# Kernel tuning notes

Hardware: AMD Instinct MI355X
Metric: run time of the kernel (lower is better)

The kernel has to match this reference:

```python
import jax, jax.numpy as jnp
import numpy as np

B, L, D, F = 1, 4096, 4096, 11008
# (start, end, side): side 0 = vision expert, side 1 = language expert.
# Mirrors merge_section_size over alternating contiguous vision/language token ranges.
SEGMENTS = [(0, 1024, 0), (1024, 2048, 1), (2048, 3072, 0), (3072, 4096, 1)]


def setup_inputs() -> dict:
    key = jax.random.key(0)
    ks = jax.random.split(key, 7)
    s = 0.02  # weight init scale
    hidden_states = jax.random.normal(ks[0], (B, L, D), jnp.float32)
    tt = np.zeros((B, L), np.int32)
    for a, b, side in SEGMENTS:
        tt[:, a:b] = side
    token_type_ids = jnp.asarray(tt)
    lg_w = jax.random.normal(ks[1], (D, F), jnp.float32) * s
    lu_w = jax.random.normal(ks[2], (D, F), jnp.float32) * s
    ld_w = jax.random.normal(ks[3], (F, D), jnp.float32) * s
    vg_w = jax.random.normal(ks[4], (D, F), jnp.float32) * s
    vu_w = jax.random.normal(ks[5], (D, F), jnp.float32) * s
    vd_w = jax.random.normal(ks[6], (F, D), jnp.float32) * s
    return {
        'hidden_states': hidden_states,
        'token_type_ids': token_type_ids,
        'lg_w': lg_w, 'lu_w': lu_w, 'ld_w': ld_w,
        'vg_w': vg_w, 'vu_w': vu_w, 'vd_w': vd_w,
    }


def _swiglu_mlp(x, gw, uw, dw):
    # x: [B, T, D] -> [B, T, D]; down(silu(gate(x)) * up(x))
    h = jax.nn.silu(jnp.einsum('btd,df->btf', x, gw)) * jnp.einsum('btd,df->btf', x, uw)
    return jnp.einsum('btf,fd->btd', h, dw)


def reference(hidden_states, token_type_ids, lg_w, lu_w, ld_w, vg_w, vu_w, vd_w):
    # Split-dispatch over static contiguous segments, then concat along seq dim.
    outs = []
    for a, b, side in SEGMENTS:
        seg = hidden_states[:, a:b, :]
        if side == 1:
            outs.append(_swiglu_mlp(seg, lg_w, lu_w, ld_w))
        else:
            outs.append(_swiglu_mlp(seg, vg_w, vu_w, vd_w))
    return jnp.concatenate(outs, axis=1)
```

## Files before the change

### kernel.cpp

```cpp
#include <hip/hip_runtime.h>
#include <math.h>

typedef unsigned short u16;
typedef short s16x8 __attribute__((ext_vector_type(8)));
typedef float f32x4 __attribute__((ext_vector_type(4)));

#define GLOAD16(gp, lp)                                                        \
  __builtin_amdgcn_global_load_lds(                                            \
      (const __attribute__((address_space(1))) void*)(gp),                     \
      (__attribute__((address_space(3))) void*)(lp), 16, 0, 0)

__device__ __forceinline__ u16 f2bf(float f) {
  union { float f; unsigned u; } v; v.f = f;
  unsigned r = v.u + 0x7fffu + ((v.u >> 16) & 1u);
  return (u16)(r >> 16);
}

__global__ __launch_bounds__(256) void cvt_x_kernel(const float* __restrict__ in,
                                                    u16* __restrict__ out) {
  size_t i = ((size_t)blockIdx.x * 256 + threadIdx.x) * 8;
  float4 a = *(const float4*)(in + i);
  float4 b = *(const float4*)(in + i + 4);
  s16x8 v;
  v[0] = (short)f2bf(a.x); v[1] = (short)f2bf(a.y);
  v[2] = (short)f2bf(a.z); v[3] = (short)f2bf(a.w);
  v[4] = (short)f2bf(b.x); v[5] = (short)f2bf(b.y);
  v[6] = (short)f2bf(b.z); v[7] = (short)f2bf(b.w);
  *(s16x8*)(out + i) = v;
}

__global__ __launch_bounds__(256) void transpose_cvt_kernel(
    const float* __restrict__ in0, const float* __restrict__ in1,
    const float* __restrict__ in2, const float* __restrict__ in3,
    const float* __restrict__ in4, const float* __restrict__ in5,
    u16* __restrict__ o01, u16* __restrict__ o23,
    u16* __restrict__ o4, u16* __restrict__ o5) {
  __shared__ float s[64 * 65];
  const int mat = blockIdx.y;
  const float* in; u16* out;
  switch (mat) {
    case 0: in = in0; out = o01; break;
    case 1: in = in1; out = o01; break;
    case 2: in = in2; out = o23; break;
    case 3: in = in3; out = o23; break;
    case 4: in = in4; out = o4; break;
    default: in = in5; out = o5; break;
  }
  const int R = (mat < 4) ? 4096 : 11008;
  const int C = (mat < 4) ? 11008 : 4096;
  const int nTc = C >> 6;
  const int tr = blockIdx.x / nTc, tc = blockIdx.x - tr * nTc;
  const int r0 = tr << 6, c0 = tc << 6;
  const int t = threadIdx.x;
#pragma unroll
  for (int p = 0; p < 4; ++p) {
    const int lr = p * 16 + (t >> 4);
    const int lc = (t & 15) * 4;
    float4 v = *(const float4*)(in + (size_t)(r0 + lr) * C + (c0 + lc));
    float* sp = &s[lr * 65 + lc];
    sp[0] = v.x; sp[1] = v.y; sp[2] = v.z; sp[3] = v.w;
  }
  __syncthreads();
#pragma unroll
  for (int q = 0; q < 2; ++q) {
    const int oc = q * 32 + (t >> 3);
    const int orr = (t & 7) * 8;
    s16x8 v;
#pragma unroll
    for (int i = 0; i < 8; ++i) v[i] = (short)f2bf(s[(orr + i) * 65 + oc]);
    const int f = c0 + oc;
    size_t orow;
    if (mat < 4) orow = (size_t)((f >> 4) << 5) + ((mat & 1) << 4) + (f & 15);
    else         orow = (size_t)f;
    *(s16x8*)(out + orow * R + (r0 + orr)) = v;
  }
}

template <int KB, int EPI>
__global__ __launch_bounds__(512, 1) void gemm256(
    const u16* __restrict__ A, const u16* __restrict__ Bl,
    const u16* __restrict__ Bv, const int* __restrict__ tt,
    void* __restrict__ OutP) {
  constexpr int NK = KB / 128;
  constexpr int L = NK / 2;
  __shared__ u16 sA[2][2][128][64];
  __shared__ u16 sB[2][2][128][64];

  const int nwg = gridDim.x;
  const int bid = blockIdx.x;
  const int wg = (bid & 7) * (nwg >> 3) + (bid >> 3);
  const int mT = wg & 15;
  const int nT = wg >> 4;

  const int t = threadIdx.x;
  const int lane = t & 63;
  const int rlo = lane & 15;
  const int hi = lane >> 4;
  const int wn = (t >> 6) & 3;
  const int wm = (t >> 8) & 1;

  const int side = tt[mT << 8];
  const u16* B = side ? Bl : Bv;

  const int rowq = t >> 3;
  const int gsw = ((t & 7) ^ (rowq & 7)) << 4;
  const char* srcA = (const char*)A + (size_t)(mT * 256 + rowq) * KB + gsw;
  const char* srcB = (const char*)B + (size_t)(nT * 256 + rowq) * KB + gsw;
  char* ldsA = (char*)&sA[0][0][0][0];
  char* ldsB = (char*)&sB[0][0][0][0];
  const int woff = (t & 448) << 4;

#define STG_A(d, h, kt)                                                        \
  do {                                                                         \
    GLOAD16(srcA + (size_t)((h) * 128) * KB + (kt) * 128,                      \
            ldsA + (d) * 32768 + (h) * 16384 + woff);                          \
    GLOAD16(srcA + (size_t)((h) * 128 + 64) * KB + (kt) * 128,                 \
            ldsA + (d) * 32768 + (h) * 16384 + 8192 + woff);                   \
  } while (0)
#define STG_B(d, h, kt)                                                        \
  do {                                                                         \
    GLOAD16(srcB + (size_t)((h) * 128) * KB + (kt) * 128,                      \
            ldsB + (d) * 32768 + (h) * 16384 + woff);                          \
    GLOAD16(srcB + (size_t)((h) * 128 + 64) * KB + (kt) * 128,                 \
            ldsB + (d) * 32768 + (h) * 16384 + 8192 + woff);                   \
  } while (0)

  const int cxa = (hi ^ (rlo & 7)) << 4;
  const int cxb = ((4 + hi) ^ (rlo & 7)) << 4;
  const int arow = (wm * 64 + rlo) * 128;
  const int brow = (wn * 32 + rlo) * 128;

  s16x8 af[4][2], bf[2][2];
  f32x4 acc[8][4];
  const f32x4 z = {0.f, 0.f, 0.f, 0.f};
#pragma unroll
  for (int i = 0; i < 8; ++i)
#pragma unroll
    for (int j = 0; j < 4; ++j) acc[i][j] = z;

#define LDA(d, mh)                                                             \
  do {                                                                         \
    _Pragma("unroll") for (int fi = 0; fi < 4; ++fi) {                         \
      const char* p = ldsA + (d) * 32768 + (mh) * 16384 + arow + fi * 2048;    \
      af[fi][0] = *(const s16x8*)(p + cxa);                                    \
      af[fi][1] = *(const s16x8*)(p + cxb);                                    \
    }                                                                          \
  } while (0)
#define LDB(d, nh)                                                             \
  do {                                                                         \
    _Pragma("unroll") for (int gi = 0; gi < 2; ++gi) {                         \
      const char* p = ldsB + (d) * 32768 + (nh) * 16384 + brow + gi * 2048;    \
      bf[gi][0] = *(const s16x8*)(p + cxa);                                    \
      bf[gi][1] = *(const s16x8*)(p + cxb);                                    \
    }                                                                          \
  } while (0)
#define MFMA16(mh, nh)                                                         \
  do {                                                                         \
    __builtin_amdgcn_s_setprio(1);                                             \
    _Pragma("unroll") for (int fi = 0; fi < 4; ++fi)                           \
        _Pragma("unroll") for (int gi = 0; gi < 2; ++gi) {                     \
      acc[(mh)*4 + fi][(nh)*2 + gi] = __builtin_amdgcn_mfma_f32_16x16x32_bf16( \
          af[fi][0], bf[gi][0], acc[(mh)*4 + fi][(nh)*2 + gi], 0, 0, 0);       \
      acc[(mh)*4 + fi][(nh)*2 + gi] = __builtin_amdgcn_mfma_f32_16x16x32_bf16( \
          af[fi][1], bf[gi][1], acc[(mh)*4 + fi][(nh)*2 + gi], 0, 0, 0);       \
    }                                                                          \
    __builtin_amdgcn_s_setprio(0);                                             \
  } while (0)
#define SBAR() __builtin_amdgcn_s_barrier()
#define LGKM0() asm volatile("s_waitcnt lgkmcnt(0)")
#define LGKM8() asm volatile("s_waitcnt lgkmcnt(8)")
#define VMCNT6() asm volatile("s_waitcnt vmcnt(6)")
#define VMCNT0() asm volatile("s_waitcnt vmcnt(0)")

  STG_A(0, 0, 0); STG_B(0, 0, 0); STG_A(0, 1, 0); STG_B(0, 1, 0);
  STG_B(1, 0, 1); STG_A(1, 1, 1); STG_B(1, 1, 1);
  VMCNT6();
  SBAR();

  for (int it = 0; it < L - 1; ++it) {
    const int T = 2 * it;
    LDA(0, 0); LDB(0, 0);
    STG_A(1, 0, T + 1);
    LGKM8();
    SBAR(); LGKM0(); MFMA16(0, 0); SBAR();
    LDA(0, 1);
    STG_B(0, 0, T + 2);
    SBAR(); LGKM0(); MFMA16(1, 0); SBAR();
    LDB(0, 1);
    STG_A(0, 1, T + 2);
    SBAR(); LGKM0(); MFMA16(1, 1); SBAR();
    LDA(0, 0);
    STG_B(0, 1, T + 2);
    VMCNT6();
    SBAR(); LGKM0(); MFMA16(0, 1); SBAR();
    LDA(1, 0); LDB(1, 0);
    STG_A(0, 0, T + 2);
    LGKM8();
    SBAR(); LGKM0(); MFMA16(0, 0); SBAR();
    LDA(1, 1);
    STG_B(1, 0, T + 3);
    SBAR(); LGKM0(); MFMA16(1, 0); SBAR();
    LDB(1, 1);
    STG_A(1, 1, T + 3);
    SBAR(); LGKM0(); MFMA16(1, 1); SBAR();
    LDA(1, 0);
    STG_B(1, 1, T + 3);
    VMCNT6();
    SBAR(); LGKM0(); MFMA16(0, 1); SBAR();
  }
  {
    const int T = NK - 2;
    LDA(0, 0); LDB(0, 0);
    STG_A(1, 0, T + 1);
    LGKM8();
    SBAR(); LGKM0(); MFMA16(0, 0); SBAR();
    LDA(0, 1);
    SBAR(); LGKM0(); MFMA16(1, 0); SBAR();
    LDB(0, 1);
    SBAR(); LGKM0(); MFMA16(1, 1); SBAR();
    LDA(0, 0);
    VMCNT0();
    SBAR(); LGKM0(); MFMA16(0, 1); SBAR();
    LDA(1, 0); LDB(1, 0);
    LGKM8();
    SBAR(); LGKM0(); MFMA16(0, 0); SBAR();
    LDA(1, 1);
    SBAR(); LGKM0(); MFMA16(1, 0); SBAR();
    LDB(1, 1);
    SBAR(); LGKM0(); MFMA16(1, 1); SBAR();
    LDA(1, 0);
    SBAR(); LGKM0(); MFMA16(0, 1);
  }

  if (EPI == 0) {
    u16* H = (u16*)OutP;
#pragma unroll
    for (int mh = 0; mh < 2; ++mh)
#pragma unroll
      for (int fi = 0; fi < 4; ++fi) {
        const int row0 = mT * 256 + mh * 128 + wm * 64 + fi * 16 + hi * 4;
#pragma unroll
        for (int nh = 0; nh < 2; ++nh) {
          const int fc = nT * 128 + (nh * 4 + wn) * 16 + rlo;
          const f32x4 g = acc[mh * 4 + fi][nh * 2 + 0];
          const f32x4 u = acc[mh * 4 + fi][nh * 2 + 1];
#pragma unroll
          for (int r = 0; r < 4; ++r) {
            const float gv = g[r];
            const float hv = gv / (1.f + __expf(-gv)) * u[r];
            H[(size_t)(row0 + r) * 11008 + fc] = f2bf(hv);
          }
        }
      }
  } else {
    float* O = (float*)OutP;
#pragma unroll
    for (int mh = 0; mh < 2; ++mh)
#pragma unroll
      for (int fi = 0; fi < 4; ++fi) {
        const int row0 = mT * 256 + mh * 128 + wm * 64 + fi * 16 + hi * 4;
#pragma unroll
        for (int nh = 0; nh < 2; ++nh)
#pragma unroll
          for (int gi = 0; gi < 2; ++gi) {
            const int col = nT * 256 + nh * 128 + wn * 32 + gi * 16 + rlo;
            const f32x4 a = acc[mh * 4 + fi][nh * 2 + gi];
#pragma unroll
            for (int r = 0; r < 4; ++r)
              O[(size_t)(row0 + r) * 4096 + col] = a[r];
          }
      }
  }
#undef STG_A
#undef STG_B
#undef LDA
#undef LDB
#undef MFMA16
#undef SBAR
#undef LGKM0
#undef LGKM8
#undef VMCNT6
#undef VMCNT0
}

extern "C" void kernel_launch(void* const* d_in, const int* in_sizes, int n_in,
                              void* d_out, int out_size, void* d_ws, size_t ws_size,
                              hipStream_t stream) {
  (void)in_sizes; (void)n_in; (void)out_size; (void)ws_size;
  const float* x  = (const float*)d_in[0];
  const int*   tt = (const int*)d_in[1];
  const float* lg = (const float*)d_in[2];
  const float* lu = (const float*)d_in[3];
  const float* ld = (const float*)d_in[4];
  const float* vg = (const float*)d_in[5];
  const float* vu = (const float*)d_in[6];
  const float* vd = (const float*)d_in[7];

  u16* ws  = (u16*)d_ws;
  u16* xbf = ws;
  u16* GUl = xbf + 16777216;
  u16* GUv = GUl + 90177536;
  u16* ldT = GUv + 90177536;
  u16* vdT = ldT + 45088768;
  u16* hbuf = vdT + 45088768;

  cvt_x_kernel<<<dim3(8192), dim3(256), 0, stream>>>(x, xbf);
  transpose_cvt_kernel<<<dim3(11008, 6), dim3(256), 0, stream>>>(
      lg, lu, vg, vu, ld, vd, GUl, GUv, ldT, vdT);
  gemm256<8192, 0><<<dim3(1376), dim3(512), 0, stream>>>(xbf, GUl, GUv, tt, hbuf);
  gemm256<22016, 1><<<dim3(256), dim3(512), 0, stream>>>(hbuf, ldT, vdT, tt, d_out);
}
```

Measured before the change: 1.474 ms.

## Make gate/up GEMM persistent over 256 workgroups and reorder MFMA schedule

```diff
diff --git a/kernel.cpp b/kernel.cpp
--- a/kernel.cpp
+++ b/kernel.cpp
@@ -76,19 +76,202 @@
   }
 }
 
-template <int KB, int EPI>
-__global__ __launch_bounds__(512, 1) void gemm256(
+#define SBAR() __builtin_amdgcn_s_barrier()
+#define LGKM0() asm volatile("s_waitcnt lgkmcnt(0)")
+#define LGKM8() asm volatile("s_waitcnt lgkmcnt(8)")
+#define VMCNT6() asm volatile("s_waitcnt vmcnt(6)")
+#define VMCNT0() asm volatile("s_waitcnt vmcnt(0)")
+
+__global__ __launch_bounds__(512, 1) void gemm_gateup_persist(
     const u16* __restrict__ A, const u16* __restrict__ Bl,
     const u16* __restrict__ Bv, const int* __restrict__ tt,
-    void* __restrict__ OutP) {
-  constexpr int NK = KB / 128;
-  constexpr int L = NK / 2;
+    u16* __restrict__ H) {
   __shared__ u16 sA[2][2][128][64];
   __shared__ u16 sB[2][2][128][64];
 
-  const int nwg = gridDim.x;
   const int bid = blockIdx.x;
-  const int wg = (bid & 7) * (nwg >> 3) + (bid >> 3);
+  const int c = ((bid >> 7) << 3) | (bid & 7);
+  const int mT = (bid >> 3) & 15;
+  const int ntiles = (c < 6) ? 6 : 5;
+  const int FK = ntiles * 64;
+
+  const int t = threadIdx.x;
+  const int lane = t & 63;
+  const int rlo = lane & 15;
+  const int hi = lane >> 4;
+  const int wn = (t >> 6) & 3;
+  const int wm = (t >> 8) & 1;
+
+  const int side = tt[mT << 8];
+  const u16* B = side ? Bl : Bv;
+
+  const int rowq = t >> 3;
+  const int gsw = ((t & 7) ^ (rowq & 7)) << 4;
+  const char* srcA = (const char*)A + (size_t)(mT * 256 + rowq) * 8192 + gsw;
+  const char* srcB0 = (const char*)B + ((size_t)(c * 256) + rowq) * 8192 + gsw;
+  char* ldsA = (char*)&sA[0][0][0][0];
+  char* ldsB = (char*)&sB[0][0][0][0];
+  const int woff = (t & 448) << 4;
+
+#define PSTG_A(d, h, q)                                                        \
+  do {                                                                         \
+    const char* _pa = srcA + ((q) & 63) * 128;                                 \
+    GLOAD16(_pa + (size_t)((h) * 128) * 8192,                                  \
+            ldsA + (d) * 32768 + (h) * 16384 + woff);                          \
+    GLOAD16(_pa + (size_t)((h) * 128 + 64) * 8192,                             \
+            ldsA + (d) * 32768 + (h) * 16384 + 8192 + woff);                   \
+  } while (0)
+#define PSTG_B(d, h, q)                                                        \
+  do {                                                                         \
+    const char* _pb = srcB0 + (size_t)((q) >> 6) * 33554432 +                  \
+                      (size_t)((h) * 128) * 8192 + ((q) & 63) * 128;           \
+    GLOAD16(_pb, ldsB + (d) * 32768 + (h) * 16384 + woff);                     \
+    GLOAD16(_pb + (size_t)64 * 8192,                                           \
+            ldsB + (d) * 32768 + (h) * 16384 + 8192 + woff);                   \
+  } while (0)
+
+  const int cxa = (hi ^ (rlo & 7)) << 4;
+  const int cxb = ((4 + hi) ^ (rlo & 7)) << 4;
+  const int arow = (wm * 64 + rlo) * 128;
+  const int brow = (wn * 32 + rlo) * 128;
+
+  s16x8 af[4][2], bf[2][2][2];
+  f32x4 acc[8][4];
+  const f32x4 z = {0.f, 0.f, 0.f, 0.f};
+#pragma unroll
+  for (int i = 0; i < 8; ++i)
+#pragma unroll
+    for (int j = 0; j < 4; ++j) acc[i][j] = z;
+
+#define LDA(d, mh)                                                             \
+  do {                                                                         \
+    _Pragma("unroll") for (int fi = 0; fi < 4; ++fi) {                         \
+      const char* p = ldsA + (d) * 32768 + (mh) * 16384 + arow + fi * 2048;    \
+      af[fi][0] = *(const s16x8*)(p + cxa);                                    \
+      af[fi][1] = *(const s16x8*)(p + cxb);                                    \
+    }                                                                          \
+  } while (0)
+#define LDBS(bi, d, nh)                                                        \
+  do {                                                                         \
+    _Pragma("unroll") for (int gi = 0; gi < 2; ++gi) {                         \
+      const char* p = ldsB + (d) * 32768 + (nh) * 16384 + brow + gi * 2048;    \
+      bf[bi][gi][0] = *(const s16x8*)(p + cxa);                                \
+      bf[bi][gi][1] = *(const s16x8*)(p + cxb);                                \
+    }                                                                          \
+  } while (0)
+#define MFMA16(mh, nh)                                                         \
+  do {                                                                         \
+    __builtin_amdgcn_s_setprio(1);                                             \
+    _Pragma("unroll") for (int fi = 0; fi < 4; ++fi)                           \
+        _Pragma("unroll") for (int gi = 0; gi < 2; ++gi) {                     \
+      acc[(mh)*4 + fi][(nh)*2 + gi] = __builtin_amdgcn_mfma_f32_16x16x32_bf16( \
+          af[fi][0], bf[nh][gi][0], acc[(mh)*4 + fi][(nh)*2 + gi], 0, 0, 0);   \
+      acc[(mh)*4 + fi][(nh)*2 + gi] = __builtin_amdgcn_mfma_f32_16x16x32_bf16( \
+          af[fi][1], bf[nh][gi][1], acc[(mh)*4 + fi][(nh)*2 + gi], 0, 0, 0);   \
+    }                                                                          \
+    __builtin_amdgcn_s_setprio(0);                                             \
+  } while (0)
+
+#define GU_EPI(nTv)                                                            \
+  do {                                                                         \
+    const int _nT = (nTv);                                                     \
+    _Pragma("unroll") for (int mh = 0; mh < 2; ++mh)                           \
+        _Pragma("unroll") for (int fi = 0; fi < 4; ++fi) {                     \
+      const int row0 = mT * 256 + mh * 128 + wm * 64 + fi * 16 + hi * 4;       \
+      _Pragma("unroll") for (int nh = 0; nh < 2; ++nh) {                       \
+        const int fc = _nT * 128 + (nh * 4 + wn) * 16 + rlo;                   \
+        const f32x4 g = acc[mh * 4 + fi][nh * 2 + 0];                          \
+        const f32x4 u = acc[mh * 4 + fi][nh * 2 + 1];                          \
+        _Pragma("unroll") for (int r = 0; r < 4; ++r) {                        \
+          const float gv = g[r];                                               \
+          const float hv = gv / (1.f + __expf(-gv)) * u[r];                    \
+          H[(size_t)(row0 + r) * 11008 + fc] = f2bf(hv);                       \
+        }                                                                      \
+      }                                                                        \
+    }                                                                          \
+  } while (0)
+
+  PSTG_A(0, 0, 0); PSTG_B(0, 0, 0); PSTG_B(0, 1, 0); PSTG_A(0, 1, 0);
+  PSTG_A(1, 0, 1); PSTG_B(1, 0, 1); PSTG_B(1, 1, 1);
+  VMCNT6();
+  SBAR();
+
+  for (int T = 0; T < FK - 2; T += 2) {
+    LDA(0, 0); LDBS(0, 0, 0);
+    PSTG_A(1, 1, T + 1);
+    LGKM8();
+    SBAR(); LGKM0(); MFMA16(0, 0); SBAR();
+    LDBS(1, 0, 1);
+    PSTG_A(0, 0, T + 2);
+    SBAR(); LGKM0(); MFMA16(0, 1); SBAR();
+    LDA(0, 1);
+    PSTG_B(0, 0, T + 2);
+    SBAR(); LGKM0(); MFMA16(1, 1); SBAR();
+    PSTG_B(0, 1, T + 2);
+    VMCNT6();
+    SBAR(); MFMA16(1, 0); SBAR();
+    LDA(1, 0); LDBS(0, 1, 0);
+    PSTG_A(0, 1, T + 2);
+    LGKM8();
+    SBAR(); LGKM0(); MFMA16(0, 0); SBAR();
+    LDBS(1, 1, 1);
+    PSTG_A(1, 0, T + 3);
+    SBAR(); LGKM0(); MFMA16(0, 1); SBAR();
+    LDA(1, 1);
+    PSTG_B(1, 0, T + 3);
+    SBAR(); LGKM0(); MFMA16(1, 1); SBAR();
+    PSTG_B(1, 1, T + 3);
+    VMCNT6();
+    SBAR(); MFMA16(1, 0); SBAR();
+
+    if ((T & 63) == 62) {
+      GU_EPI(c + 16 * (T >> 6));
+#pragma unroll
+      for (int i = 0; i < 8; ++i)
+#pragma unroll
+        for (int j = 0; j < 4; ++j) acc[i][j] = z;
+    }
+  }
+  {
+    LDA(0, 0); LDBS(0, 0, 0);
+    PSTG_A(1, 1, FK - 1);
+    LGKM8();
+    SBAR(); LGKM0(); MFMA16(0, 0); SBAR();
+    LDBS(1, 0, 1);
+    SBAR(); LGKM0(); MFMA16(0, 1); SBAR();
+    LDA(0, 1);
+    SBAR(); LGKM0(); MFMA16(1, 1); SBAR();
+    VMCNT0();
+    SBAR(); MFMA16(1, 0); SBAR();
+    LDA(1, 0); LDBS(0, 1, 0);
+    LGKM8();
+    SBAR(); LGKM0(); MFMA16(0, 0); SBAR();
+    LDBS(1, 1, 1);
+    SBAR(); LGKM0(); MFMA16(0, 1); SBAR();
+    LDA(1, 1);
+    SBAR(); LGKM0(); MFMA16(1, 1); SBAR();
+    MFMA16(1, 0);
+  }
+  GU_EPI(c + 16 * (ntiles - 1));
+#undef PSTG_A
+#undef PSTG_B
+#undef LDA
+#undef LDBS
+#undef MFMA16
+#undef GU_EPI
+}
+
+__global__ __launch_bounds__(512, 1) void gemm_down(
+    const u16* __restrict__ A, const u16* __restrict__ Bl,
+    const u16* __restrict__ Bv, const int* __restrict__ tt,
+    float* __restrict__ O) {
+  constexpr int KB = 22016;
+  constexpr int NK = KB / 128;
+  __shared__ u16 sA[2][2][128][64];
+  __shared__ u16 sB[2][2][128][64];
+
+  const int bid = blockIdx.x;
+  const int wg = (bid & 7) * 32 + (bid >> 3);
   const int mT = wg & 15;
   const int nT = wg >> 4;
 
@@ -130,7 +313,7 @@
   const int arow = (wm * 64 + rlo) * 128;
   const int brow = (wn * 32 + rlo) * 128;
 
-  s16x8 af[4][2], bf[2][2];
+  s16x8 af[4][2], bf[2][2][2];
   f32x4 acc[8][4];
   const f32x4 z = {0.f, 0.f, 0.f, 0.f};
 #pragma unroll
@@ -146,12 +329,12 @@
       af[fi][1] = *(const s16x8*)(p + cxb);                                    \
     }                                                                          \
   } while (0)
-#define LDB(d, nh)                                                             \
+#define LDBS(bi, d, nh)                                                        \
   do {                                                                         \
     _Pragma("unroll") for (int gi = 0; gi < 2; ++gi) {                         \
       const char* p = ldsB + (d) * 32768 + (nh) * 16384 + brow + gi * 2048;    \
-      bf[gi][0] = *(const s16x8*)(p + cxa);                                    \
-      bf[gi][1] = *(const s16x8*)(p + cxb);                                    \
+      bf[bi][gi][0] = *(const s16x8*)(p + cxa);                                \
+      bf[bi][gi][1] = *(const s16x8*)(p + cxb);                                \
     }                                                                          \
   } while (0)
 #define MFMA16(mh, nh)                                                         \
@@ -160,127 +343,88 @@
     _Pragma("unroll") for (int fi = 0; fi < 4; ++fi)                           \
         _Pragma("unroll") for (int gi = 0; gi < 2; ++gi) {                     \
       acc[(mh)*4 + fi][(nh)*2 + gi] = __builtin_amdgcn_mfma_f32_16x16x32_bf16( \
-          af[fi][0], bf[gi][0], acc[(mh)*4 + fi][(nh)*2 + gi], 0, 0, 0);       \
+          af[fi][0], bf[nh][gi][0], acc[(mh)*4 + fi][(nh)*2 + gi], 0, 0, 0);   \
       acc[(mh)*4 + fi][(nh)*2 + gi] = __builtin_amdgcn_mfma_f32_16x16x32_bf16( \
-          af[fi][1], bf[gi][1], acc[(mh)*4 + fi][(nh)*2 + gi], 0, 0, 0);       \
+          af[fi][1], bf[nh][gi][1], acc[(mh)*4 + fi][(nh)*2 + gi], 0, 0, 0);   \
     }                                                                          \
     __builtin_amdgcn_s_setprio(0);                                             \
   } while (0)
-#define SBAR() __builtin_amdgcn_s_barrier()
-#define LGKM0() asm volatile("s_waitcnt lgkmcnt(0)")
-#define LGKM8() asm volatile("s_waitcnt lgkmcnt(8)")
-#define VMCNT6() asm volatile("s_waitcnt vmcnt(6)")
-#define VMCNT0() asm volatile("s_waitcnt vmcnt(0)")
-
-  STG_A(0, 0, 0); STG_B(0, 0, 0); STG_A(0, 1, 0); STG_B(0, 1, 0);
-  STG_B(1, 0, 1); STG_A(1, 1, 1); STG_B(1, 1, 1);
+
+  STG_A(0, 0, 0); STG_B(0, 0, 0); STG_B(0, 1, 0); STG_A(0, 1, 0);
+  STG_A(1, 0, 1); STG_B(1, 0, 1); STG_B(1, 1, 1);
   VMCNT6();
   SBAR();
 
-  for (int it = 0; it < L - 1; ++it) {
-    const int T = 2 * it;
-    LDA(0, 0); LDB(0, 0);
-    STG_A(1, 0, T + 1);
-    LGKM8();
-    SBAR(); LGKM0(); MFMA16(0, 0); SBAR();
+  for (int T = 0; T < NK - 2; T += 2) {
+    LDA(0, 0); LDBS(0, 0, 0);
+    STG_A(1, 1, T + 1);
+    LGKM8();
+    SBAR(); LGKM0(); MFMA16(0, 0); SBAR();
+    LDBS(1, 0, 1);
+    STG_A(0, 0, T + 2);
+    SBAR(); LGKM0(); MFMA16(0, 1); SBAR();
     LDA(0, 1);
     STG_B(0, 0, T + 2);
-    SBAR(); LGKM0(); MFMA16(1, 0); SBAR();
-    LDB(0, 1);
-    STG_A(0, 1, T + 2);
-    SBAR(); LGKM0(); MFMA16(1, 1); SBAR();
-    LDA(0, 0);
+    SBAR(); LGKM0(); MFMA16(1, 1); SBAR();
     STG_B(0, 1, T + 2);
     VMCNT6();
-    SBAR(); LGKM0(); MFMA16(0, 1); SBAR();
-    LDA(1, 0); LDB(1, 0);
-    STG_A(0, 0, T + 2);
-    LGKM8();
-    SBAR(); LGKM0(); MFMA16(0, 0); SBAR();
+    SBAR(); MFMA16(1, 0); SBAR();
+    LDA(1, 0); LDBS(0, 1, 0);
+    STG_A(0, 1, T + 2);
+    LGKM8();
+    SBAR(); LGKM0(); MFMA16(0, 0); SBAR();
+    LDBS(1, 1, 1);
+    STG_A(1, 0, T + 3);
+    SBAR(); LGKM0(); MFMA16(0, 1); SBAR();
     LDA(1, 1);
     STG_B(1, 0, T + 3);
-    SBAR(); LGKM0(); MFMA16(1, 0); SBAR();
-    LDB(1, 1);
-    STG_A(1, 1, T + 3);
-    SBAR(); LGKM0(); MFMA16(1, 1); SBAR();
-    LDA(1, 0);
+    SBAR(); LGKM0(); MFMA16(1, 1); SBAR();
     STG_B(1, 1, T + 3);
     VMCNT6();
-    SBAR(); LGKM0(); MFMA16(0, 1); SBAR();
+    SBAR(); MFMA16(1, 0); SBAR();
   }
   {
-    const int T = NK - 2;
-    LDA(0, 0); LDB(0, 0);
-    STG_A(1, 0, T + 1);
-    LGKM8();
-    SBAR(); LGKM0(); MFMA16(0, 0); SBAR();
+    LDA(0, 0); LDBS(0, 0, 0);
+    STG_A(1, 1, NK - 1);
+    LGKM8();
+    SBAR(); LGKM0(); MFMA16(0, 0); SBAR();
+    LDBS(1, 0, 1);
+    SBAR(); LGKM0(); MFMA16(0, 1); SBAR();
     LDA(0, 1);
-    SBAR(); LGKM0(); MFMA16(1, 0); SBAR();
-    LDB(0, 1);
-    SBAR(); LGKM0(); MFMA16(1, 1); SBAR();
-    LDA(0, 0);
+    SBAR(); LGKM0(); MFMA16(1, 1); SBAR();
     VMCNT0();
-    SBAR(); LGKM0(); MFMA16(0, 1); SBAR();
-    LDA(1, 0); LDB(1, 0);
-    LGKM8();
-    SBAR(); LGKM0(); MFMA16(0, 0); SBAR();
+    SBAR(); MFMA16(1, 0); SBAR();
+    LDA(1, 0); LDBS(0, 1, 0);
+    LGKM8();
+    SBAR(); LGKM0(); MFMA16(0, 0); SBAR();
+    LDBS(1, 1, 1);
+    SBAR(); LGKM0(); MFMA16(0, 1); SBAR();
     LDA(1, 1);
-    SBAR(); LGKM0(); MFMA16(1, 0); SBAR();
-    LDB(1, 1);
-    SBAR(); LGKM0(); MFMA16(1, 1); SBAR();
-    LDA(1, 0);
-    SBAR(); LGKM0(); MFMA16(0, 1);
-  }
-
-  if (EPI == 0) {
-    u16* H = (u16*)OutP;
-#pragma unroll
-    for (int mh = 0; mh < 2; ++mh)
-#pragma unroll
-      for (int fi = 0; fi < 4; ++fi) {
-        const int row0 = mT * 256 + mh * 128 + wm * 64 + fi * 16 + hi * 4;
-#pragma unroll
-        for (int nh = 0; nh < 2; ++nh) {
-          const int fc = nT * 128 + (nh * 4 + wn) * 16 + rlo;
-          const f32x4 g = acc[mh * 4 + fi][nh * 2 + 0];
-          const f32x4 u = acc[mh * 4 + fi][nh * 2 + 1];
-#pragma unroll
-          for (int r = 0; r < 4; ++r) {
-            const float gv = g[r];
-            const float hv = gv / (1.f + __expf(-gv)) * u[r];
-            H[(size_t)(row0 + r) * 11008 + fc] = f2bf(hv);
-          }
+    SBAR(); LGKM0(); MFMA16(1, 1); SBAR();
+    MFMA16(1, 0);
+  }
+
+#pragma unroll
+  for (int mh = 0; mh < 2; ++mh)
+#pragma unroll
+    for (int fi = 0; fi < 4; ++fi) {
+      const int row0 = mT * 256 + mh * 128 + wm * 64 + fi * 16 + hi * 4;
+#pragma unroll
+      for (int nh = 0; nh < 2; ++nh)
+#pragma unroll
+        for (int gi = 0; gi < 2; ++gi) {
+          const int col = nT * 256 + nh * 128 + wn * 32 + gi * 16 + rlo;
+          const f32x4 a = acc[mh * 4 + fi][nh * 2 + gi];
+#pragma unroll
+          for (int r = 0; r < 4; ++r)
+            O[(size_t)(row0 + r) * 4096 + col] = a[r];
         }
-      }
-  } else {
-    float* O = (float*)OutP;
-#pragma unroll
-    for (int mh = 0; mh < 2; ++mh)
-#pragma unroll
-      for (int fi = 0; fi < 4; ++fi) {
-        const int row0 = mT * 256 + mh * 128 + wm * 64 + fi * 16 + hi * 4;
-#pragma unroll
-        for (int nh = 0; nh < 2; ++nh)
-#pragma unroll
-          for (int gi = 0; gi < 2; ++gi) {
-            const int col = nT * 256 + nh * 128 + wn * 32 + gi * 16 + rlo;
-            const f32x4 a = acc[mh * 4 + fi][nh * 2 + gi];
-#pragma unroll
-            for (int r = 0; r < 4; ++r)
-              O[(size_t)(row0 + r) * 4096 + col] = a[r];
-          }
-      }
-  }
+    }
 #undef STG_A
 #undef STG_B
 #undef LDA
-#undef LDB
+#undef LDBS
 #undef MFMA16
-#undef SBAR
-#undef LGKM0
-#undef LGKM8
-#undef VMCNT6
-#undef VMCNT0
 }
 
 extern "C" void kernel_launch(void* const* d_in, const int* in_sizes, int n_in,
@@ -307,6 +451,7 @@
   cvt_x_kernel<<<dim3(8192), dim3(256), 0, stream>>>(x, xbf);
   transpose_cvt_kernel<<<dim3(11008, 6), dim3(256), 0, stream>>>(
       lg, lu, vg, vu, ld, vd, GUl, GUv, ldT, vdT);
-  gemm256<8192, 0><<<dim3(1376), dim3(512), 0, stream>>>(xbf, GUl, GUv, tt, hbuf);
-  gemm256<22016, 1><<<dim3(256), dim3(512), 0, stream>>>(hbuf, ldT, vdT, tt, d_out);
-}
+  gemm_gateup_persist<<<dim3(256), dim3(512), 0, stream>>>(
+      xbf, GUl, GUv, tt, hbuf);
+  gemm_down<<<dim3(256), dim3(512), 0, stream>>>(hbuf, ldT, vdT, tt, (float*)d_out);
+}
```

Result: faster. 1.309 ms (-11.2%).
